# Kernel optimization log

Hardware: AMD Instinct MI355X
Metric: run time of the kernel (lower is better)

The kernel has to match this reference:

```python
import jax, jax.numpy as jnp
import numpy as np

B, T_IN, T_OUT, N, FEAT = 32, 96, 96, 512, 8
HID = 512
GRID_SIZE, SPLINE_ORDER = 5, 3
GRID_RANGE = (-1.0, 1.0)


def _make_grid():
    # matches KANLinear.create_grid: identical row per in_feature, so keep 1-D
    h = (GRID_RANGE[1] - GRID_RANGE[0]) / GRID_SIZE
    return jnp.arange(-SPLINE_ORDER, GRID_SIZE + SPLINE_ORDER + 1, dtype=jnp.float32) * h + GRID_RANGE[0]


def _b_splines(x, grid):
    # x: [M, in_features]; de Boor-Cox recursion, order SPLINE_ORDER
    x = x[..., None]  # [M, in, 1]
    bases = ((x >= grid[:-1]) & (x < grid[1:])).astype(x.dtype)
    for k in range(1, SPLINE_ORDER + 1):
        left = (x - grid[:-(k + 1)]) / (grid[k:-1] - grid[:-(k + 1)])
        right = (grid[k + 1:] - x) / (grid[k + 1:] - grid[1:-k])
        bases = left * bases[..., :-1] + right * bases[..., 1:]
    return bases  # [M, in, grid_size + spline_order]


def setup_inputs() -> dict:
    key = jax.random.key(0)
    ks = jax.random.split(key, 12)
    s = 0.05
    return {
        "X": jax.random.normal(ks[0], (B, T_IN, N, FEAT), jnp.float32),
        "Y": jax.random.normal(ks[1], (B, T_OUT, N, FEAT), jnp.float32),
        "Wx": jax.random.normal(ks[2], (HID, T_IN * FEAT), jnp.float32) * s,
        "bx": jax.random.normal(ks[3], (HID,), jnp.float32) * s,
        "Wy": jax.random.normal(ks[4], (HID, T_OUT * FEAT), jnp.float32) * s,
        "by": jax.random.normal(ks[5], (HID,), jnp.float32) * s,
        "base_w": jax.random.normal(ks[6], (64, 2 * HID), jnp.float32) * s,
        "spline_w": jax.random.normal(ks[7], (64, 2 * HID, GRID_SIZE + SPLINE_ORDER), jnp.float32) * s,
        "spline_scaler": jax.random.normal(ks[8], (64, 2 * HID), jnp.float32) * s,
        "Wf": jax.random.normal(ks[9], (T_OUT * FEAT, 64), jnp.float32) * s,
        "bf": jax.random.normal(ks[10], (T_OUT * FEAT,), jnp.float32) * s,
    }


def reference(X, Y, Wx, bx, Wy, by, base_w, spline_w, spline_scaler, Wf, bf):
    # [B, T, N, F] -> [B, N, T*F]
    Xf = jnp.transpose(X, (0, 2, 1, 3)).reshape(B, N, T_IN * FEAT)
    Yf = jnp.transpose(Y, (0, 2, 1, 3)).reshape(B, N, T_OUT * FEAT)
    Hx = jnp.tanh(Xf @ Wx.T + bx)
    Hy = jnp.tanh(Yf @ Wy.T + by)
    h = jnp.concatenate([Hx, Hy], axis=-1).reshape(B * N, 2 * HID)

    grid = _make_grid()
    base_out = jax.nn.silu(h) @ base_w.T
    scaled_sw = spline_w * spline_scaler[..., None]  # [out, in, coeff]
    spline_out = jnp.einsum("mik,oik->mo", _b_splines(h, grid), scaled_sw)
    kan_out = (base_out + spline_out).reshape(B, N, 64)

    out = kan_out @ Wf.T + bf  # [B, N, T_OUT*FEAT]
    out = out.reshape(B, N, T_OUT, FEAT)
    return jnp.transpose(out, (0, 2, 1, 3))  # [B, T_OUT, N, FEAT]
```

## Files before the change

kernel.cpp:

```cpp
#include <hip/hip_runtime.h>
#include <cmath>

#define B_    32
#define T_    96
#define N_    512
#define F_    8
#define TF_   768
#define HID_  512
#define M_    16384
#define KIN_  1024
#define KS_   8

typedef short short8 __attribute__((ext_vector_type(8)));
typedef _Float16 halfx8 __attribute__((ext_vector_type(8)));
typedef float f32x4  __attribute__((ext_vector_type(4)));
typedef unsigned int  uintx4 __attribute__((ext_vector_type(4)));
typedef unsigned long long ulongx2 __attribute__((ext_vector_type(2)));
typedef unsigned short      ushort_t;
typedef unsigned int        uint_t;
typedef unsigned long long  ulong_t;

#define HT_B     0ull
#define WQ_B     33554432ull
#define WB_B     34734080ull
#define SH_B     36306944ull
#define KANR_B   61472768ull
#define WFQ_B    63569920ull

static __device__ inline uint_t  fbits(float f){ return __builtin_bit_cast(uint_t, f); }
static __device__ inline ushort_t f2b(float f){
    uint_t u = fbits(f);
    return (ushort_t)((u + 0x7fffu + ((u >> 16) & 1u)) >> 16);
}
static __device__ inline float b2f(ushort_t h){ return __builtin_bit_cast(float, (uint_t)h << 16); }
static __device__ inline ulong_t pack4(float4 v){
    return (ulong_t)f2b(v.x) | ((ulong_t)f2b(v.y) << 16) |
           ((ulong_t)f2b(v.z) << 32) | ((ulong_t)f2b(v.w) << 48);
}
static __device__ inline ulong_t pack4t(float4 v){
    uint_t d0 = (fbits(v.x) >> 16) | (fbits(v.y) & 0xffff0000u);
    uint_t d1 = (fbits(v.z) >> 16) | (fbits(v.w) & 0xffff0000u);
    return (ulong_t)d0 | ((ulong_t)d1 << 32);
}
static __device__ inline float fast_tanh(float x){
    const float e = __expf(2.0f * x);
    return 1.0f - 2.0f / (e + 1.0f);
}
static __device__ inline void gload_lds16(const void* g, void* l){
    __builtin_amdgcn_global_load_lds(
        (const __attribute__((address_space(1))) unsigned int*)g,
        (__attribute__((address_space(3))) unsigned int*)l, 16, 0, 0);
}

__global__ __launch_bounds__(256) void pack_wq(
    const float* __restrict__ base_w,
    const float* __restrict__ spline_w,
    const float* __restrict__ scaler,
    ushort_t* __restrict__ wq)
{
    const int e = blockIdx.x * 256 + threadIdx.x;
    const int j    = e & 7;
    const int ln   = (e >> 3) & 63;
    const int ct   = (e >> 9) & 3;
    const int t    = (e >> 11) & 3;
    const int rest = e >> 13;
    const int ss   = rest % 9;
    const int ks   = rest / 9;
    const int o = ct * 16 + (ln & 15);
    const int g = ln >> 4;
    float v;
    if (ss < 8) {
        const int i = ks * 128 + ss * 16 + t * 4 + g;
        v = spline_w[(o * KIN_ + i) * 8 + j] * scaler[o * KIN_ + i];
    } else {
        const int i = ks * 128 + t * 32 + g * 8 + j;
        v = base_w[o * KIN_ + i];
    }
    wq[e] = f2b(v);
}

__global__ __launch_bounds__(256) void pack_wb2(
    const float* __restrict__ Wx,
    const float* __restrict__ Wy,
    ushort_t* __restrict__ wb)
{
    const int e = blockIdx.x * 256 + threadIdx.x;
    const float v = (e < 512 * TF_) ? Wx[e] : Wy[e - 512 * TF_];
    wb[e] = f2b(v);
}

__global__ __launch_bounds__(256) void pack_wfq(
    const float* __restrict__ Wf, ushort_t* __restrict__ wfq)
{
    const int e = blockIdx.x * 256 + threadIdx.x;
    const int jj  = e & 7;
    const int ln  = (e >> 3) & 63;
    const int rt  = (e >> 9) & 3;
    const int s   = (e >> 11) & 1;
    const int wvt = (e >> 12) & 1;
    const int tb  = e >> 13;
    const int tf = tb * 128 + wvt * 64 + rt * 16 + (ln & 15);
    const int o  = s * 32 + (ln >> 4) * 8 + jj;
    wfq[e] = f2b(Wf[(size_t)tf * 64 + o]);
}

__global__ __launch_bounds__(256) void xcvt_kernel(
    const float* __restrict__ Xs, ushort_t* __restrict__ xbf)
{
    __shared__ __align__(16) char lds[32 * 1552];
    const int tid = threadIdx.x;
    const int n0  = blockIdx.x * 32;
    const int bb  = blockIdx.y;
    const int nl  = (tid & 63) >> 1;
    const int f4  = (tid & 1) * 4;
    const int tq  = tid >> 6;
    #pragma unroll 4
    for (int u = 0; u < 24; u++) {
        const int t = u * 4 + tq;
        const float4 v = *(const float4*)(Xs + (size_t)bb * (T_ * N_ * F_)
                                             + (size_t)t * (N_ * F_)
                                             + (size_t)(n0 + nl) * F_ + f4);
        *(ulong_t*)(lds + nl * 1552 + t * 16 + f4 * 2) = pack4t(v);
    }
    __syncthreads();
    #pragma unroll 4
    for (int u = 0; u < 12; u++) {
        const int c   = u * 256 + tid;
        const int row = c / 96;
        const int col = c - row * 96;
        const uintx4 val = *(const uintx4*)(lds + row * 1552 + col * 16);
        *(uintx4*)(xbf + (size_t)(bb * 512 + n0 + row) * TF_ + col * 8) = val;
    }
}

__global__ __launch_bounds__(512, 2) void gemm_tanh_v7(
    const ushort_t* __restrict__ xbf,
    const ushort_t* __restrict__ wb,
    const float* __restrict__ bias,
    ushort_t* __restrict__ ht, int z)
{
    __shared__ __align__(16) char smem[32768];

    const int tid = threadIdx.x;
    const int wv  = tid >> 6;
    const int ln  = tid & 63;
    const int lr  = ln & 15;
    const int hi  = ln >> 4;
    const int wm  = wv >> 2;
    const int wj  = wv & 3;

    const int m0  = blockIdx.x * 128;
    const int jl0 = blockIdx.y * 128;
    const int j0  = z * 512 + jl0;

    const int r_l = ln >> 3;
    const int ck  = ((ln & 7) ^ r_l) * 8;

    f32x4 acc[4][2] = {};

    for (int kt = 0; kt < 12; kt++) {
        __syncthreads();
        #pragma unroll
        for (int s = 0; s < 2; s++) {
            const int reg = s * 8 + wv;
            const int row = reg * 8 + r_l;
            gload_lds16(xbf + (size_t)(m0 + row) * TF_ + kt * 64 + ck,
                        smem + reg * 1024 + ln * 16);
            gload_lds16(wb + (size_t)(j0 + row) * TF_ + kt * 64 + ck,
                        smem + 16384 + reg * 1024 + ln * 16);
        }
        __syncthreads();

        #pragma unroll
        for (int h = 0; h < 2; h++) {
            const int g = h * 4 + hi;
            short8 a[4], b[2];
            #pragma unroll
            for (int rt = 0; rt < 4; rt++) {
                const int r = wm * 64 + rt * 16 + lr;
                a[rt] = *(short8*)(smem + r * 128 + ((g ^ (r & 7)) * 16));
            }
            #pragma unroll
            for (int ct = 0; ct < 2; ct++) {
                const int r = wj * 32 + ct * 16 + lr;
                b[ct] = *(short8*)(smem + 16384 + r * 128 + ((g ^ (r & 7)) * 16));
            }
            #pragma unroll
            for (int rt = 0; rt < 4; rt++)
                #pragma unroll
                for (int ct = 0; ct < 2; ct++)
                    acc[rt][ct] = __builtin_amdgcn_mfma_f32_16x16x32_bf16(
                        a[rt], b[ct], acc[rt][ct], 0, 0, 0);
        }
    }

    __syncthreads();
    #pragma unroll
    for (int ct = 0; ct < 2; ct++) {
        const int j = wj * 32 + ct * 16 + lr;
        const float bvv = bias[jl0 + j];
        #pragma unroll
        for (int rt = 0; rt < 4; rt++) {
            const f32x4 v = acc[rt][ct];
            float4 tv;
            tv.x = fast_tanh(v[0] + bvv);
            tv.y = fast_tanh(v[1] + bvv);
            tv.z = fast_tanh(v[2] + bvv);
            tv.w = fast_tanh(v[3] + bvv);
            const int slot = wm * 8 + rt * 2 + (hi >> 1);
            *(ulong_t*)(smem + j * 256 + ((slot ^ (j & 15)) * 16) + (hi & 1) * 8)
                = pack4(tv);
        }
    }
    __syncthreads();
    {
        const int j  = tid >> 2;
        const int q4 = tid & 3;
        ushort_t* dst = ht + (size_t)(j0 + j) * M_ + m0 + q4 * 32;
        #pragma unroll
        for (int w = 0; w < 4; w++) {
            const int slot = q4 * 4 + w;
            short8 val = *(short8*)(smem + j * 256 + ((slot ^ (j & 15)) * 16));
            *(short8*)(dst + w * 8) = val;
        }
    }
}

static __device__ inline short8 eval_bases(float x)
{
    const float v = fmaf(x, 2.5f, 2.5f);
    float sf = floorf(v);
    sf = fminf(sf, 4.0f);
    const float u = v - sf;
    const int si = (int)sf;
    const float u2 = u * u, u3 = u2 * u;
    const float omu = 1.0f - u;
    const float omu3 = omu * omu * omu;
    const float Bb0 = omu3 * (1.0f / 6.0f);
    const float Bb3 = u3 * (1.0f / 6.0f);
    const float Bb1 = fmaf(0.5f, u3, 2.0f / 3.0f) - u2;
    const float Bb2 = 1.0f - Bb0 - Bb1 - Bb3;
    const uint_t d0 = (fbits(Bb0) >> 16) | (fbits(Bb1) & 0xffff0000u);
    const uint_t d1 = (fbits(Bb2) >> 16) | (fbits(Bb3) & 0xffff0000u);
    const ulong_t P = (ulong_t)d0 | ((ulong_t)d1 << 32);
    const int sh = si << 4;
    const ulong_t Plo = P << (sh & 63);
    const ulong_t Phi = P >> ((64 - sh) & 63);
    ulongx2 pr;
    pr.x = (si == 4) ? 0ull : Plo;
    pr.y = (si == 0) ? 0ull : ((si == 4) ? P : Phi);
    return __builtin_bit_cast(short8, pr);
}

__global__ __launch_bounds__(256) void kan_v8(
    const ushort_t* __restrict__ ht,
    const ushort_t* __restrict__ wq,
    _Float16* __restrict__ kanp)
{
    __shared__ __align__(16) char lds[40960];

    const int tid = threadIdx.x;
    const int wv  = tid >> 6;
    const int ln  = tid & 63;
    const int g   = ln >> 4;
    const int lr  = ln & 15;
    const int m0  = blockIdx.x * 128;
    const int ks  = blockIdx.y;
    const int iB  = ks * 128;

    const ushort_t* wqk = wq + (size_t)ks * 73728;

    #pragma unroll
    for (int c = 0; c < 8; c++) {
        const int ll = wv * 8 + c;
        const int il = ll * 4 + (ln >> 4);
        const int r8 = (ln & 15) * 8;
        gload_lds16(ht + (size_t)(iB + il) * M_ + m0 + r8,
                    lds + ll * 1024 + ln * 16);
    }
    gload_lds16(wqk + (size_t)wv * 512 + ln * 8,
                lds + 32768 + wv * 1024 + ln * 16);
    __syncthreads();

    const int hbA = g * 256  + wv * 64 + lr * 2;
    const int hbS = g * 2048 + wv * 64 + lr * 2;

    f32x4 acc[2][4] = {};

    #pragma unroll
    for (int it = 0; it < 36; ++it) {
        const int p = it & 1;
        char* sb = lds + 32768 + p * 4096;
        const short8 b0 = *(short8*)(sb + 0 * 1024 + ln * 16);
        const short8 b1 = *(short8*)(sb + 1 * 1024 + ln * 16);
        const short8 b2 = *(short8*)(sb + 2 * 1024 + ln * 16);
        const short8 b3 = *(short8*)(sb + 3 * 1024 + ln * 16);

        if (it < 35)
            gload_lds16(wqk + (size_t)((it + 1) * 4 + wv) * 512 + ln * 8,
                        lds + 32768 + (p ^ 1) * 4096 + wv * 1024 + ln * 16);

        short8 a0, a1;
        if (it < 32) {
            const int off = hbA + ((it >> 2) * 16 + (it & 3) * 4) * 256;
            a0 = eval_bases(b2f(*(const ushort_t*)(lds + off)));
            a1 = eval_bases(b2f(*(const ushort_t*)(lds + off + 32)));
        } else {
            const int t = it - 32;
            uintx4 d0v, d1v;
            #pragma unroll
            for (int jj = 0; jj < 4; jj++) {
                const int o0 = hbS + (t * 32 + 2 * jj) * 256;
                const int o1 = o0 + 256;
                const float x0 = b2f(*(const ushort_t*)(lds + o0));
                const float x1 = b2f(*(const ushort_t*)(lds + o1));
                const float y0 = b2f(*(const ushort_t*)(lds + o0 + 32));
                const float y1 = b2f(*(const ushort_t*)(lds + o1 + 32));
                const float s0 = x0 / (1.0f + __expf(-x0));
                const float s1 = x1 / (1.0f + __expf(-x1));
                const float u0 = y0 / (1.0f + __expf(-y0));
                const float u1 = y1 / (1.0f + __expf(-y1));
                d0v[jj] = (fbits(s0) >> 16) | (fbits(s1) & 0xffff0000u);
                d1v[jj] = (fbits(u0) >> 16) | (fbits(u1) & 0xffff0000u);
            }
            a0 = __builtin_bit_cast(short8, d0v);
            a1 = __builtin_bit_cast(short8, d1v);
        }

        acc[0][0] = __builtin_amdgcn_mfma_f32_16x16x32_bf16(a0, b0, acc[0][0], 0, 0, 0);
        acc[0][1] = __builtin_amdgcn_mfma_f32_16x16x32_bf16(a0, b1, acc[0][1], 0, 0, 0);
        acc[0][2] = __builtin_amdgcn_mfma_f32_16x16x32_bf16(a0, b2, acc[0][2], 0, 0, 0);
        acc[0][3] = __builtin_amdgcn_mfma_f32_16x16x32_bf16(a0, b3, acc[0][3], 0, 0, 0);
        acc[1][0] = __builtin_amdgcn_mfma_f32_16x16x32_bf16(a1, b0, acc[1][0], 0, 0, 0);
        acc[1][1] = __builtin_amdgcn_mfma_f32_16x16x32_bf16(a1, b1, acc[1][1], 0, 0, 0);
        acc[1][2] = __builtin_amdgcn_mfma_f32_16x16x32_bf16(a1, b2, acc[1][2], 0, 0, 0);
        acc[1][3] = __builtin_amdgcn_mfma_f32_16x16x32_bf16(a1, b3, acc[1][3], 0, 0, 0);

        __syncthreads();
    }

    #pragma unroll
    for (int rt = 0; rt < 2; rt++) {
        #pragma unroll
        for (int ct = 0; ct < 4; ct++) {
            const int o = ct * 16 + lr;
            #pragma unroll
            for (int q = 0; q < 4; q++) {
                const size_t row = (size_t)(m0 + wv * 32 + rt * 16 + g * 4 + q);
                kanp[(size_t)ks * (M_ * 64) + row * 64 + o] = (_Float16)acc[rt][ct][q];
            }
        }
    }
}

__global__ __launch_bounds__(256) void reduce_kan(
    const _Float16* __restrict__ kanp, ushort_t* __restrict__ kanr)
{
    const int e8 = blockIdx.x * 256 + threadIdx.x;
    const size_t base = (size_t)e8 * 8;
    float s[8] = {};
    #pragma unroll
    for (int p = 0; p < KS_; p++) {
        const halfx8 v = *(const halfx8*)(kanp + (size_t)p * (M_ * 64) + base);
        #pragma unroll
        for (int j = 0; j < 8; j++) s[j] += (float)v[j];
    }
    float4 s0 = make_float4(s[0], s[1], s[2], s[3]);
    float4 s1 = make_float4(s[4], s[5], s[6], s[7]);
    ulongx2 outv;
    outv.x = pack4(s0);
    outv.y = pack4(s1);
    *(ulongx2*)(kanr + base) = outv;
}

__global__ __launch_bounds__(256) void final_v2(
    const ushort_t* __restrict__ kanr,
    const ushort_t* __restrict__ wfq,
    const float* __restrict__ bf,
    float* __restrict__ out)
{
    const int tid = threadIdx.x;
    const int wv  = tid >> 6;
    const int ln  = tid & 63;
    const int lr  = ln & 15;
    const int hi  = ln >> 4;
    const int wvm = wv >> 1;
    const int wvt = wv & 1;
    const int mb  = blockIdx.x;
    const int tb  = blockIdx.y;

    f32x4 acc[4][4] = {};

    #pragma unroll
    for (int s = 0; s < 2; s++) {
        short8 afr[4], bfr[4];
        #pragma unroll
        for (int rt = 0; rt < 4; rt++) {
            const size_t idx = ((size_t)(((tb * 2 + wvt) * 2 + s) * 4 + rt)) * 64 + ln;
            afr[rt] = ((const short8*)wfq)[idx];
        }
        #pragma unroll
        for (int ct = 0; ct < 4; ct++) {
            const int m = mb * 128 + wvm * 64 + ct * 16 + lr;
            bfr[ct] = *(const short8*)(kanr + (size_t)m * 64 + s * 32 + hi * 8);
        }
        #pragma unroll
        for (int rt = 0; rt < 4; rt++)
            #pragma unroll
            for (int ct = 0; ct < 4; ct++)
                acc[rt][ct] = __builtin_amdgcn_mfma_f32_16x16x32_bf16(
                    afr[rt], bfr[ct], acc[rt][ct], 0, 0, 0);
    }

    #pragma unroll
    for (int rt = 0; rt < 4; rt++) {
        const int tf0 = tb * 128 + wvt * 64 + rt * 16 + hi * 4;
        const float4 b4 = *(const float4*)&bf[tf0];
        const int t  = tf0 >> 3;
        const int f0 = tf0 & 7;
        #pragma unroll
        for (int ct = 0; ct < 4; ct++) {
            const int m = mb * 128 + wvm * 64 + ct * 16 + lr;
            const int bb = m >> 9;
            const int n  = m & 511;
            const f32x4 v = acc[rt][ct];
            float4 o4 = make_float4(v[0] + b4.x, v[1] + b4.y, v[2] + b4.z, v[3] + b4.w);
            *(float4*)&out[(size_t)bb * (T_ * N_ * F_)
                           + (size_t)t * (N_ * F_)
                           + (size_t)n * F_ + f0] = o4;
        }
    }
}

extern "C" void kernel_launch(void* const* d_in, const int* in_sizes, int n_in,
                              void* d_out, int out_size, void* d_ws, size_t ws_size,
                              hipStream_t stream)
{
    const float* X      = (const float*)d_in[0];
    const float* Y      = (const float*)d_in[1];
    const float* Wx     = (const float*)d_in[2];
    const float* bx     = (const float*)d_in[3];
    const float* Wy     = (const float*)d_in[4];
    const float* by     = (const float*)d_in[5];
    const float* base_w = (const float*)d_in[6];
    const float* spline_w = (const float*)d_in[7];
    const float* spline_scaler = (const float*)d_in[8];
    const float* Wf     = (const float*)d_in[9];
    const float* bf     = (const float*)d_in[10];

    float* out = (float*)d_out;
    ushort_t* ht   = (ushort_t*)((char*)d_ws + HT_B);
    ushort_t* wq   = (ushort_t*)((char*)d_ws + WQ_B);
    ushort_t* wb   = (ushort_t*)((char*)d_ws + WB_B);
    ushort_t* xbf  = (ushort_t*)((char*)d_ws + SH_B);
    _Float16* kanp = (_Float16*)((char*)d_ws + SH_B);
    ushort_t* kanr = (ushort_t*)((char*)d_ws + KANR_B);
    ushort_t* wfq  = (ushort_t*)((char*)d_ws + WFQ_B);

    pack_wq<<<2304, 256, 0, stream>>>(base_w, spline_w, spline_scaler, wq);
    pack_wb2<<<3072, 256, 0, stream>>>(Wx, Wy, wb);
    pack_wfq<<<192, 256, 0, stream>>>(Wf, wfq);

    xcvt_kernel<<<dim3(16, 32), 256, 0, stream>>>(X, xbf);
    gemm_tanh_v7<<<dim3(128, 4), 512, 0, stream>>>(xbf, wb, bx, ht, 0);
    xcvt_kernel<<<dim3(16, 32), 256, 0, stream>>>(Y, xbf);
    gemm_tanh_v7<<<dim3(128, 4), 512, 0, stream>>>(xbf, wb, by, ht, 1);

    kan_v8<<<dim3(M_ / 128, KS_), 256, 0, stream>>>(ht, wq, kanp);
    reduce_kan<<<512, 256, 0, stream>>>(kanp, kanr);
    final_v2<<<dim3(128, 6), 256, 0, stream>>>(kanr, wfq, bf, out);
}
```

Before: 138.7 us.

## Swizzle KAN LDS tile, register-prefetch weights, split spline and base loops

The KAN kernel now loads the hidden-activation tile into LDS with an XOR swizzle so per-lane scalar reads hit fewer bank conflicts, and the base_w packing is reordered to match the new layout. Weight tiles are prefetched two iterations ahead into registers and written to the double-buffered LDS slot, replacing per-iteration async global-to-LDS loads. The loop is split into a 32-iteration spline loop with paired (vectorised) B-spline evaluation and a separate 4-iteration SiLU/base loop, which removes the branch. This adds register pressure and exposes global-load latency through registers, in exchange for simpler addressing and fewer LDS conflicts.

```diff
diff --git a/kernel.cpp b/kernel.cpp
--- a/kernel.cpp
+++ b/kernel.cpp
@@ -14,6 +14,7 @@
 typedef short short8 __attribute__((ext_vector_type(8)));
 typedef _Float16 halfx8 __attribute__((ext_vector_type(8)));
 typedef float f32x4  __attribute__((ext_vector_type(4)));
+typedef float f32x2  __attribute__((ext_vector_type(2)));
 typedef unsigned int  uintx4 __attribute__((ext_vector_type(4)));
 typedef unsigned long long ulongx2 __attribute__((ext_vector_type(2)));
 typedef unsigned short      ushort_t;
@@ -73,7 +74,7 @@
         const int i = ks * 128 + ss * 16 + t * 4 + g;
         v = spline_w[(o * KIN_ + i) * 8 + j] * scaler[o * KIN_ + i];
     } else {
-        const int i = ks * 128 + t * 32 + g * 8 + j;
+        const int i = ks * 128 + t * 32 + j * 4 + g;
         v = base_w[o * KIN_ + i];
     }
     wq[e] = f2b(v);
@@ -226,22 +227,10 @@
     }
 }
 
-static __device__ inline short8 eval_bases(float x)
-{
-    const float v = fmaf(x, 2.5f, 2.5f);
-    float sf = floorf(v);
-    sf = fminf(sf, 4.0f);
-    const float u = v - sf;
-    const int si = (int)sf;
-    const float u2 = u * u, u3 = u2 * u;
-    const float omu = 1.0f - u;
-    const float omu3 = omu * omu * omu;
-    const float Bb0 = omu3 * (1.0f / 6.0f);
-    const float Bb3 = u3 * (1.0f / 6.0f);
-    const float Bb1 = fmaf(0.5f, u3, 2.0f / 3.0f) - u2;
-    const float Bb2 = 1.0f - Bb0 - Bb1 - Bb3;
-    const uint_t d0 = (fbits(Bb0) >> 16) | (fbits(Bb1) & 0xffff0000u);
-    const uint_t d1 = (fbits(Bb2) >> 16) | (fbits(Bb3) & 0xffff0000u);
+static __device__ inline short8 shift_pack(float b0, float b1, float b2, float b3, int si)
+{
+    const uint_t d0 = (fbits(b0) >> 16) | (fbits(b1) & 0xffff0000u);
+    const uint_t d1 = (fbits(b2) >> 16) | (fbits(b3) & 0xffff0000u);
     const ulong_t P = (ulong_t)d0 | ((ulong_t)d1 << 32);
     const int sh = si << 4;
     const ulong_t Plo = P << (sh & 63);
@@ -252,7 +241,26 @@
     return __builtin_bit_cast(short8, pr);
 }
 
-__global__ __launch_bounds__(256) void kan_v8(
+static __device__ inline void eval_bases2(float x0, float x1, short8& a0, short8& a1)
+{
+    f32x2 x = {x0, x1};
+    f32x2 v = x * 2.5f + 2.5f;
+    f32x2 sf = __builtin_elementwise_floor(v);
+    sf = __builtin_elementwise_min(sf, (f32x2){4.0f, 4.0f});
+    const f32x2 u  = v - sf;
+    const f32x2 u2 = u * u;
+    const f32x2 u3 = u2 * u;
+    const f32x2 omu = 1.0f - u;
+    const f32x2 omu3 = omu * omu * omu;
+    const f32x2 B0 = omu3 * (1.0f / 6.0f);
+    const f32x2 B3 = u3 * (1.0f / 6.0f);
+    const f32x2 B1 = (u3 * 0.5f + (2.0f / 3.0f)) - u2;
+    const f32x2 B2 = 1.0f - B0 - B1 - B3;
+    a0 = shift_pack(B0[0], B1[0], B2[0], B3[0], (int)sf[0]);
+    a1 = shift_pack(B0[1], B1[1], B2[1], B3[1], (int)sf[1]);
+}
+
+__global__ __launch_bounds__(256) void kan_v9(
     const ushort_t* __restrict__ ht,
     const ushort_t* __restrict__ wq,
     _Float16* __restrict__ kanp)
@@ -274,58 +282,34 @@
     for (int c = 0; c < 8; c++) {
         const int ll = wv * 8 + c;
         const int il = ll * 4 + (ln >> 4);
-        const int r8 = (ln & 15) * 8;
-        gload_lds16(ht + (size_t)(iB + il) * M_ + m0 + r8,
-                    lds + ll * 1024 + ln * 16);
+        const int chunk = ln & 15;
+        const int rowst = (chunk ^ ((il & 3) << 1)) * 8;
+        gload_lds16(ht + (size_t)(iB + il) * M_ + m0 + rowst,
+                    lds + ll * 1024 + (ln & 15) * 16 + (ln >> 4) * 256);
     }
     gload_lds16(wqk + (size_t)wv * 512 + ln * 8,
                 lds + 32768 + wv * 1024 + ln * 16);
+    short8 wA = *(const short8*)(wqk + (size_t)(1 * 4 + wv) * 512 + ln * 8);
+    short8 wB = *(const short8*)(wqk + (size_t)(2 * 4 + wv) * 512 + ln * 8);
     __syncthreads();
 
-    const int hbA = g * 256  + wv * 64 + lr * 2;
-    const int hbS = g * 2048 + wv * 64 + lr * 2;
+    const int hb0 = g * 256 + ((wv * 64 + lr * 2) ^ (g << 5));
+    const int hb1 = g * 256 + ((wv * 64 + 32 + lr * 2) ^ (g << 5));
 
     f32x4 acc[2][4] = {};
 
-    #pragma unroll
-    for (int it = 0; it < 36; ++it) {
-        const int p = it & 1;
-        char* sb = lds + 32768 + p * 4096;
-        const short8 b0 = *(short8*)(sb + 0 * 1024 + ln * 16);
-        const short8 b1 = *(short8*)(sb + 1 * 1024 + ln * 16);
-        const short8 b2 = *(short8*)(sb + 2 * 1024 + ln * 16);
-        const short8 b3 = *(short8*)(sb + 3 * 1024 + ln * 16);
-
-        if (it < 35)
-            gload_lds16(wqk + (size_t)((it + 1) * 4 + wv) * 512 + ln * 8,
-                        lds + 32768 + (p ^ 1) * 4096 + wv * 1024 + ln * 16);
-
+    #pragma unroll 4
+    for (int it = 0; it < 32; ++it) {
+        char* rb = lds + 32768 + (it & 1) * 4096;
+        const short8 b0 = *(short8*)(rb + 0 * 1024 + ln * 16);
+        const short8 b1 = *(short8*)(rb + 1 * 1024 + ln * 16);
+        const short8 b2 = *(short8*)(rb + 2 * 1024 + ln * 16);
+        const short8 b3 = *(short8*)(rb + 3 * 1024 + ln * 16);
+
+        const float x0 = b2f(*(const ushort_t*)(lds + hb0 + it * 1024));
+        const float x1 = b2f(*(const ushort_t*)(lds + hb1 + it * 1024));
         short8 a0, a1;
-        if (it < 32) {
-            const int off = hbA + ((it >> 2) * 16 + (it & 3) * 4) * 256;
-            a0 = eval_bases(b2f(*(const ushort_t*)(lds + off)));
-            a1 = eval_bases(b2f(*(const ushort_t*)(lds + off + 32)));
-        } else {
-            const int t = it - 32;
-            uintx4 d0v, d1v;
-            #pragma unroll
-            for (int jj = 0; jj < 4; jj++) {
-                const int o0 = hbS + (t * 32 + 2 * jj) * 256;
-                const int o1 = o0 + 256;
-                const float x0 = b2f(*(const ushort_t*)(lds + o0));
-                const float x1 = b2f(*(const ushort_t*)(lds + o1));
-                const float y0 = b2f(*(const ushort_t*)(lds + o0 + 32));
-                const float y1 = b2f(*(const ushort_t*)(lds + o1 + 32));
-                const float s0 = x0 / (1.0f + __expf(-x0));
-                const float s1 = x1 / (1.0f + __expf(-x1));
-                const float u0 = y0 / (1.0f + __expf(-y0));
-                const float u1 = y1 / (1.0f + __expf(-y1));
-                d0v[jj] = (fbits(s0) >> 16) | (fbits(s1) & 0xffff0000u);
-                d1v[jj] = (fbits(u0) >> 16) | (fbits(u1) & 0xffff0000u);
-            }
-            a0 = __builtin_bit_cast(short8, d0v);
-            a1 = __builtin_bit_cast(short8, d1v);
-        }
+        eval_bases2(x0, x1, a0, a1);
 
         acc[0][0] = __builtin_amdgcn_mfma_f32_16x16x32_bf16(a0, b0, acc[0][0], 0, 0, 0);
         acc[0][1] = __builtin_amdgcn_mfma_f32_16x16x32_bf16(a0, b1, acc[0][1], 0, 0, 0);
@@ -336,7 +320,58 @@
         acc[1][2] = __builtin_amdgcn_mfma_f32_16x16x32_bf16(a1, b2, acc[1][2], 0, 0, 0);
         acc[1][3] = __builtin_amdgcn_mfma_f32_16x16x32_bf16(a1, b3, acc[1][3], 0, 0, 0);
 
+        *(short8*)(lds + 32768 + ((it + 1) & 1) * 4096 + wv * 1024 + ln * 16) = wA;
+        wA = wB;
+        wB = *(const short8*)(wqk + (size_t)((it + 3) * 4 + wv) * 512 + ln * 8);
         __syncthreads();
+    }
+
+    #pragma unroll
+    for (int t = 0; t < 4; ++t) {
+        const int it = 32 + t;
+        char* rb = lds + 32768 + (it & 1) * 4096;
+        const short8 b0 = *(short8*)(rb + 0 * 1024 + ln * 16);
+        const short8 b1 = *(short8*)(rb + 1 * 1024 + ln * 16);
+        const short8 b2 = *(short8*)(rb + 2 * 1024 + ln * 16);
+        const short8 b3 = *(short8*)(rb + 3 * 1024 + ln * 16);
+
+        uintx4 d0v, d1v;
+        #pragma unroll
+        for (int jw = 0; jw < 4; jw++) {
+            const int o0 = hb0 + t * 8192 + (jw * 2) * 1024;
+            const int o1 = hb0 + t * 8192 + (jw * 2 + 1) * 1024;
+            const int p0 = hb1 + t * 8192 + (jw * 2) * 1024;
+            const int p1 = hb1 + t * 8192 + (jw * 2 + 1) * 1024;
+            const float x00 = b2f(*(const ushort_t*)(lds + o0));
+            const float x01 = b2f(*(const ushort_t*)(lds + o1));
+            const float x10 = b2f(*(const ushort_t*)(lds + p0));
+            const float x11 = b2f(*(const ushort_t*)(lds + p1));
+            const float s00 = x00 / (1.0f + __expf(-x00));
+            const float s01 = x01 / (1.0f + __expf(-x01));
+            const float s10 = x10 / (1.0f + __expf(-x10));
+            const float s11 = x11 / (1.0f + __expf(-x11));
+            d0v[jw] = (fbits(s00) >> 16) | (fbits(s01) & 0xffff0000u);
+            d1v[jw] = (fbits(s10) >> 16) | (fbits(s11) & 0xffff0000u);
+        }
+        const short8 a0 = __builtin_bit_cast(short8, d0v);
+        const short8 a1 = __builtin_bit_cast(short8, d1v);
+
+        acc[0][0] = __builtin_amdgcn_mfma_f32_16x16x32_bf16(a0, b0, acc[0][0], 0, 0, 0);
+        acc[0][1] = __builtin_amdgcn_mfma_f32_16x16x32_bf16(a0, b1, acc[0][1], 0, 0, 0);
+        acc[0][2] = __builtin_amdgcn_mfma_f32_16x16x32_bf16(a0, b2, acc[0][2], 0, 0, 0);
+        acc[0][3] = __builtin_amdgcn_mfma_f32_16x16x32_bf16(a0, b3, acc[0][3], 0, 0, 0);
+        acc[1][0] = __builtin_amdgcn_mfma_f32_16x16x32_bf16(a1, b0, acc[1][0], 0, 0, 0);
+        acc[1][1] = __builtin_amdgcn_mfma_f32_16x16x32_bf16(a1, b1, acc[1][1], 0, 0, 0);
+        acc[1][2] = __builtin_amdgcn_mfma_f32_16x16x32_bf16(a1, b2, acc[1][2], 0, 0, 0);
+        acc[1][3] = __builtin_amdgcn_mfma_f32_16x16x32_bf16(a1, b3, acc[1][3], 0, 0, 0);
+
+        if (t < 3) {
+            *(short8*)(lds + 32768 + ((it + 1) & 1) * 4096 + wv * 1024 + ln * 16) = wA;
+            wA = wB;
+            if (t == 0)
+                wB = *(const short8*)(wqk + (size_t)(35 * 4 + wv) * 512 + ln * 8);
+            __syncthreads();
+        }
     }
 
     #pragma unroll
@@ -466,7 +501,7 @@
     xcvt_kernel<<<dim3(16, 32), 256, 0, stream>>>(Y, xbf);
     gemm_tanh_v7<<<dim3(128, 4), 512, 0, stream>>>(xbf, wb, by, ht, 1);
 
-    kan_v8<<<dim3(M_ / 128, KS_), 256, 0, stream>>>(ht, wq, kanp);
+    kan_v9<<<dim3(M_ / 128, KS_), 256, 0, stream>>>(ht, wq, kanp);
     reduce_kan<<<512, 256, 0, stream>>>(kanp, kanr);
     final_v2<<<dim3(128, 6), 256, 0, stream>>>(kanr, wfq, bf, out);
 }
```

Result: no change. 137.1 us (-1.1%).
